# Kernel tuning notes

Hardware: AMD Instinct MI355X
Metric: run time of the kernel (lower is better)

The kernel has to match this reference:

```python
import jax, jax.numpy as jnp
import numpy as np

N = 20000
E = 320000
IN_C, HID, OUT_C = 128, 64, 32
H12, H3 = 4, 1  # heads for conv1/conv2 and conv3
NEG_SLOPE = 0.2


def _glorot(key, shape):
    fan_in, fan_out = shape[0], shape[-1]
    lim = (6.0 / (fan_in + fan_out)) ** 0.5
    return jax.random.uniform(key, shape, jnp.float32, -lim, lim)


def setup_inputs() -> dict:
    key = jax.random.key(0)
    ks = jax.random.split(key, 16)
    x = jax.random.normal(ks[0], (N, IN_C), jnp.float32)
    edge_index = jax.random.randint(ks[1], (2, E), 0, N, jnp.int64)
    p = {
        'W1': _glorot(ks[2], (IN_C, H12 * HID)),
        'as1': _glorot(ks[3], (H12, HID)), 'ad1': _glorot(ks[4], (H12, HID)),
        'b1': jnp.zeros((HID,), jnp.float32),
        'W2': _glorot(ks[5], (HID, H12 * HID)),
        'as2': _glorot(ks[6], (H12, HID)), 'ad2': _glorot(ks[7], (H12, HID)),
        'b2': jnp.zeros((HID,), jnp.float32),
        'W3': _glorot(ks[8], (HID, H3 * OUT_C)),
        'as3': _glorot(ks[9], (H3, OUT_C)), 'ad3': _glorot(ks[10], (H3, OUT_C)),
        'b3': jnp.zeros((OUT_C,), jnp.float32),
        'Wm': _glorot(ks[11], (OUT_C, OUT_C)), 'bm': jnp.zeros((OUT_C,), jnp.float32),
        'Wv': _glorot(ks[12], (OUT_C, OUT_C)), 'bv': jnp.zeros((OUT_C,), jnp.float32),
    }
    return dict(x=x, edge_index=edge_index, **p)


def gat_layer(x, src, dst, W, a_src, a_dst, b, heads, out_c):
    # x: [N, in_c] -> h: [N, H, C]
    h = (x @ W).reshape(-1, heads, out_c)
    alpha_s = jnp.einsum('nhc,hc->nh', h, a_src)  # [N,H]
    alpha_d = jnp.einsum('nhc,hc->nh', h, a_dst)
    e = jax.nn.leaky_relu(alpha_s[src] + alpha_d[dst], NEG_SLOPE)  # [E',H]
    # segment softmax over incoming edges of each dst node
    m = jax.ops.segment_max(e, dst, num_segments=N)
    p = jnp.exp(e - m[dst])
    s = jax.ops.segment_sum(p, dst, num_segments=N)
    alpha = p / (s[dst] + 1e-16)  # [E',H]
    msg = h[src] * alpha[:, :, None]  # [E',H,C]
    out = jax.ops.segment_sum(msg, dst, num_segments=N)  # [N,H,C]
    return out.mean(axis=1) + b  # concat=False -> mean over heads


def reference(x, edge_index, W1, as1, ad1, b1, W2, as2, ad2, b2,
              W3, as3, ad3, b3, Wm, bm, Wv, bv):
    # PyG GATConv default: add self loops
    loop = jnp.arange(N, dtype=edge_index.dtype)
    src = jnp.concatenate([edge_index[0], loop])
    dst = jnp.concatenate([edge_index[1], loop])

    h = jax.nn.relu(gat_layer(x, src, dst, W1, as1, ad1, b1, H12, HID))
    h = jax.nn.relu(gat_layer(h, src, dst, W2, as2, ad2, b2, H12, HID))
    z = gat_layer(h, src, dst, W3, as3, ad3, b3, H3, OUT_C)

    z_mean = z @ Wm + bm
    z_var = jnp.clip(jnp.exp(z @ Wv + bv), 1e-8, 100.0)
    return (z_mean, z_var, z)
```

## Files before the change

kernel.cpp:

```cpp
#include <hip/hip_runtime.h>
#include <hip/hip_bf16.h>

typedef unsigned short ushortT;
typedef short short8 __attribute__((ext_vector_type(8)));
typedef unsigned short ushort8v __attribute__((ext_vector_type(8)));
typedef float float4v __attribute__((ext_vector_type(4)));

constexpr int Nn   = 20000;
constexpr int Ee   = 320000;
constexpr int EP   = Ee + Nn;
constexpr float NSL = 0.2f;
constexpr int CAP  = 128;

__device__ __forceinline__ float b2f(__hip_bfloat16 v) { return __bfloat162float(v); }
__device__ __forceinline__ float bits2f(unsigned short u) {
    __hip_bfloat16 b; *(unsigned short*)&b = u; return __bfloat162float(b);
}
__device__ __forceinline__ unsigned short f2bits(float v) {
    __hip_bfloat16 b = __float2bfloat16(v); return *(unsigned short*)&b;
}
__device__ __forceinline__ float ldf(const void* p, size_t i, int bf) {
    return bf ? __bfloat162float(((const __hip_bfloat16*)p)[i])
              : ((const float*)p)[i];
}
__device__ __forceinline__ void stf(void* p, size_t i, float v, int bf) {
    if (bf) ((__hip_bfloat16*)p)[i] = __float2bfloat16(v);
    else    ((float*)p)[i] = v;
}

__device__ __forceinline__ int local_bf(const unsigned* __restrict__ xbits, int* c_sh) {
    int c = 0;
    for (int i = threadIdx.x; i < 512; i += 256) {
        unsigned e = (xbits[i] >> 7) & 0xFFu;
        if (e >= 110u && e <= 135u) ++c;
    }
    atomicAdd(c_sh, c);
    __syncthreads();
    return (*c_sh > 384) ? 1 : 0;
}

__global__ void setup_k(const int* __restrict__ ei, const unsigned* __restrict__ xbits,
                        int* __restrict__ eflag, int* __restrict__ fflag,
                        int* __restrict__ cnt,
                        const void* __restrict__ W1, const void* __restrict__ W2,
                        ushortT* __restrict__ WT1, ushortT* __restrict__ WT2) {
    const int b = blockIdx.x;
    if (b < 79) {
        int gi = b * 256 + threadIdx.x;
        if (gi < Nn) cnt[gi] = 0;
        if (b == 0) {
            __shared__ int bad, c_s;
            if (threadIdx.x == 0) { bad = 0; c_s = 0; }
            __syncthreads();
            for (int i = threadIdx.x; i < 1024; i += 256)
                if (ei[2 * i + 1] != 0) bad = 1;
            int bf = local_bf(xbits, &c_s);
            __syncthreads();
            if (threadIdx.x == 0) {
                *eflag = bad ? 0 : 1;
                *fflag = bf;
            }
        }
        return;
    }
    __shared__ int c_s;
    if (threadIdx.x == 0) c_s = 0;
    __syncthreads();
    const int bf = local_bf(xbits, &c_s);
    int idx = (b - 79) * 256 + threadIdx.x;
    if (idx < 256 * 128) {
        int j = idx >> 7, k = idx & 127;
        WT1[idx] = f2bits(ldf(W1, (size_t)k * 256 + j, bf));
    } else {
        int i2 = idx - 256 * 128;
        if (i2 < 256 * 64) {
            int j = i2 >> 6, k = i2 & 63;
            WT2[i2] = f2bits(ldf(W2, (size_t)k * 256 + j, bf));
        }
    }
}

__device__ __forceinline__ void load_edge(const int* __restrict__ ei, int sh, int e,
                                          int& si, int& di) {
    if (e < Ee) {
        si = ei[(size_t)e << sh];
        di = ei[(size_t)(Ee + e) << sh];
    } else {
        si = di = e - Ee;
    }
}

__global__ void scatter_k(const int* __restrict__ ei, const int* __restrict__ eflag,
                          int* __restrict__ cnt, int* __restrict__ csr) {
    int e = blockIdx.x * 256 + threadIdx.x;
    if (e >= EP) return;
    int sh = *eflag, si, di;
    load_edge(ei, sh, e, si, di);
    int pos = atomicAdd(cnt + di, 1);
    if (pos < CAP) csr[di * CAP + pos] = si;
}

template <int XMODE, int INC>
__global__ __launch_bounds__(256) void gemm_mfma(const void* __restrict__ xg,
                                                 const ushortT* __restrict__ WT,
                                                 ushortT* __restrict__ h,
                                                 const void* __restrict__ avs,
                                                 const void* __restrict__ avd,
                                                 float* __restrict__ as_, float* __restrict__ ad_,
                                                 const int* __restrict__ fflag) {
    constexpr int SW = INC + 8, SX = INC + 8, CPR = INC / 8;
    const int bf  = *fflag;
    const int xbf = (XMODE == 0) ? bf : 1;
    __shared__ ushortT wt_s[128 * SW];
    __shared__ ushortT xs[64 * SX];
    __shared__ float av_s[2][128];
    const int base = blockIdx.x * 64;
    const int jh   = blockIdx.y;
    const ushortT* WTg = WT + (size_t)jh * 128 * INC;
    for (int ch = threadIdx.x; ch < 128 * CPR; ch += 256) {
        int j = ch / CPR, kc = (ch - j * CPR) * 8;
        *(short8*)(wt_s + j * SW + kc) = *(const short8*)(WTg + j * INC + kc);
    }
    for (int ch = threadIdx.x; ch < 64 * CPR; ch += 256) {
        int nl = ch / CPR, kc = (ch - nl * CPR) * 8;
        int node = base + nl;
        short8 v = {0, 0, 0, 0, 0, 0, 0, 0};
        if (node < Nn) {
            if (xbf) {
                v = *(const short8*)((const ushortT*)xg + (size_t)node * INC + kc);
            } else {
                const float* xf = (const float*)xg + (size_t)node * INC + kc;
#pragma unroll
                for (int i = 0; i < 8; ++i) v[i] = (short)f2bits(xf[i]);
            }
        }
        *(short8*)(xs + nl * SX + kc) = v;
    }
    if (threadIdx.x < 128) {
        av_s[0][threadIdx.x] = ldf(avs, jh * 128 + threadIdx.x, bf);
        av_s[1][threadIdx.x] = ldf(avd, jh * 128 + threadIdx.x, bf);
    }
    __syncthreads();
    const int lane = threadIdx.x & 63, w = threadIdx.x >> 6;
    const int ln = lane & 15, quad = lane >> 4;
    float4v acc[8];
#pragma unroll
    for (int T = 0; T < 8; ++T) acc[T] = (float4v){0.f, 0.f, 0.f, 0.f};
#pragma unroll
    for (int ks = 0; ks < INC / 32; ++ks) {
        const int kb = ks * 32 + quad * 8;
        const short8 b = *(const short8*)(xs + (w * 16 + ln) * SX + kb);
#pragma unroll
        for (int T = 0; T < 8; ++T) {
            const short8 a = *(const short8*)(wt_s + (T * 16 + ln) * SW + kb);
            acc[T] = __builtin_amdgcn_mfma_f32_16x16x32_bf16(a, b, acc[T], 0, 0, 0);
        }
    }
    const int node = base + w * 16 + ln;
    const bool live = (node < Nn);
    ushortT* hn = h + (size_t)node * 256 + jh * 128;
    float pas0 = 0, pas1 = 0, pad0 = 0, pad1 = 0;
#pragma unroll
    for (int T = 0; T < 8; ++T) {
        const int jl = T * 16 + quad * 4;
        ushort4 pk;
        pk.x = f2bits(acc[T][0]); pk.y = f2bits(acc[T][1]);
        pk.z = f2bits(acc[T][2]); pk.w = f2bits(acc[T][3]);
        if (live) *(ushort4*)(hn + jl) = pk;
#pragma unroll
        for (int r = 0; r < 4; ++r) {
            const float v = acc[T][r];
            const float was = av_s[0][jl + r], wad = av_s[1][jl + r];
            if (T < 4) { pas0 = fmaf(v, was, pas0); pad0 = fmaf(v, wad, pad0); }
            else       { pas1 = fmaf(v, was, pas1); pad1 = fmaf(v, wad, pad1); }
        }
    }
#pragma unroll
    for (int off = 16; off < 64; off <<= 1) {
        pas0 += __shfl_xor(pas0, off, 64);
        pas1 += __shfl_xor(pas1, off, 64);
        pad0 += __shfl_xor(pad0, off, 64);
        pad1 += __shfl_xor(pad1, off, 64);
    }
    if (lane < 16 && live) {
        as_[node * 4 + jh * 2]     = pas0;
        as_[node * 4 + jh * 2 + 1] = pas1;
        ad_[node * 4 + jh * 2]     = pad0;
        ad_[node * 4 + jh * 2 + 1] = pad1;
    }
}

__global__ __launch_bounds__(256) void gemm_small(const ushortT* __restrict__ x,
                                                  const void* __restrict__ W,
                                                  __hip_bfloat16* __restrict__ h,
                                                  const void* __restrict__ avs,
                                                  const void* __restrict__ avd,
                                                  float* __restrict__ as_, float* __restrict__ ad_,
                                                  const int* __restrict__ fflag, int N) {
    constexpr int INC = 64, R = 32, PAD = R + 4;
    const int bf = *fflag;
    __shared__ float xsh[INC * PAD];
    int base = blockIdx.x * R;
    for (int i = threadIdx.x; i < R * INC; i += 256) {
        int rr = i / INC, kk = i - rr * INC;
        int nn = base + rr;
        xsh[kk * PAD + rr] = (nn < N) ? bits2f(x[(size_t)nn * INC + kk]) : 0.0f;
    }
    __syncthreads();
    const int jc = threadIdx.x & 31;
    const int g  = threadIdx.x >> 5;
    float acc[4] = {};
    if (bf) {
        const __hip_bfloat16* Wb = (const __hip_bfloat16*)W;
#pragma unroll 4
        for (int k = 0; k < INC; ++k) {
            float4 xv = *(const float4*)(xsh + k * PAD + g * 4);
            float w = b2f(Wb[k * 32 + jc]);
            acc[0] = fmaf(xv.x, w, acc[0]);
            acc[1] = fmaf(xv.y, w, acc[1]);
            acc[2] = fmaf(xv.z, w, acc[2]);
            acc[3] = fmaf(xv.w, w, acc[3]);
        }
    } else {
        const float* Wf = (const float*)W;
#pragma unroll 4
        for (int k = 0; k < INC; ++k) {
            float4 xv = *(const float4*)(xsh + k * PAD + g * 4);
            float w = Wf[k * 32 + jc];
            acc[0] = fmaf(xv.x, w, acc[0]);
            acc[1] = fmaf(xv.y, w, acc[1]);
            acc[2] = fmaf(xv.z, w, acc[2]);
            acc[3] = fmaf(xv.w, w, acc[3]);
        }
    }
    float avsr = ldf(avs, jc, bf), avdr = ldf(avd, jc, bf);
#pragma unroll
    for (int m = 0; m < 4; ++m) {
        int n = base + g * 4 + m;
        if (n >= N) continue;
        h[(size_t)n * 32 + jc] = __float2bfloat16(acc[m]);
        float t1 = acc[m] * avsr;
        float t2 = acc[m] * avdr;
#pragma unroll
        for (int off = 16; off > 0; off >>= 1) {
            t1 += __shfl_down(t1, off, 32);
            t2 += __shfl_down(t2, off, 32);
        }
        if (jc == 0) { as_[n] = t1; ad_[n] = t2; }
    }
}

__global__ __launch_bounds__(256) void aggr4_k(const int* __restrict__ cnt,
                                               const int* __restrict__ csr,
                                               const float* __restrict__ as_,
                                               const float* __restrict__ ad_,
                                               const unsigned short* __restrict__ h,
                                               const void* __restrict__ bias,
                                               const int* __restrict__ fflag,
                                               ushortT* __restrict__ outB, int N) {
    __shared__ float lal[4][CAP][4];
    const int lane = threadIdx.x & 63, seg = threadIdx.x >> 6;
    int d = blockIdx.x * 4 + seg;
    if (d >= N) d = N - 1;
    const int deg = min(cnt[d], CAP);
    const int base = d * CAP;
    const float4 adv = *(const float4*)(ad_ + d * 4);
    const int src0 = (lane < deg) ? csr[base + lane] : 0;
    const int src1 = (64 + lane < deg) ? csr[base + 64 + lane] : 0;
    float s0 = 0, s1 = 0, s2 = 0, s3 = 0;
    if (lane < deg) {
        float4 av = *(const float4*)(as_ + src0 * 4);
        float v0 = av.x + adv.x; v0 = v0 > 0.f ? v0 : NSL * v0; float e0 = __expf(v0);
        float v1 = av.y + adv.y; v1 = v1 > 0.f ? v1 : NSL * v1; float e1 = __expf(v1);
        float v2 = av.z + adv.z; v2 = v2 > 0.f ? v2 : NSL * v2; float e2 = __expf(v2);
        float v3 = av.w + adv.w; v3 = v3 > 0.f ? v3 : NSL * v3; float e3 = __expf(v3);
        s0 += e0; s1 += e1; s2 += e2; s3 += e3;
        *(float4*)(&lal[seg][lane][0]) = make_float4(e0, e1, e2, e3);
    }
    if (64 + lane < deg) {
        float4 av = *(const float4*)(as_ + src1 * 4);
        float v0 = av.x + adv.x; v0 = v0 > 0.f ? v0 : NSL * v0; float e0 = __expf(v0);
        float v1 = av.y + adv.y; v1 = v1 > 0.f ? v1 : NSL * v1; float e1 = __expf(v1);
        float v2 = av.z + adv.z; v2 = v2 > 0.f ? v2 : NSL * v2; float e2 = __expf(v2);
        float v3 = av.w + adv.w; v3 = v3 > 0.f ? v3 : NSL * v3; float e3 = __expf(v3);
        s0 += e0; s1 += e1; s2 += e2; s3 += e3;
        *(float4*)(&lal[seg][64 + lane][0]) = make_float4(e0, e1, e2, e3);
    }
    const int hl = lane >> 5, cl = lane & 31;
    const int q = cl >> 3, c8 = (cl & 7) * 8;
    const float* lal_s = &lal[seg][0][0];
    float a[8] = {0, 0, 0, 0, 0, 0, 0, 0};

    auto do_edge = [&](int idx, bool valid) {
        int sa = __shfl(src0, idx & 63, 64);
        int sb = __shfl(src1, idx & 63, 64);
        int src = (idx < 64) ? sa : sb;
        float ev = valid ? lal_s[idx * 4 + q] : 0.0f;
        int off = valid ? src * 256 : 0;
        ushort8v hv = *(const ushort8v*)(h + off + q * 64 + c8);
#pragma unroll
        for (int i = 0; i < 8; ++i) a[i] = fmaf(ev, bits2f(hv[i]), a[i]);
    };

    int e = 0;
    for (; e + 8 <= deg; e += 8) {
        do_edge(e + hl, true);
        do_edge(e + 2 + hl, true);
        do_edge(e + 4 + hl, true);
        do_edge(e + 6 + hl, true);
    }
    for (; e < deg; e += 2) do_edge(e + hl, (e + hl) < deg);

#pragma unroll
    for (int off = 1; off < 64; off <<= 1) {
        s0 += __shfl_xor(s0, off, 64);
        s1 += __shfl_xor(s1, off, 64);
        s2 += __shfl_xor(s2, off, 64);
        s3 += __shfl_xor(s3, off, 64);
    }
    const float sq = (q == 0) ? s0 : (q == 1) ? s1 : (q == 2) ? s2 : s3;
    const float iq = 0.25f / (sq + 1e-16f);
#pragma unroll
    for (int i = 0; i < 8; ++i) {
        a[i] *= iq;
        a[i] += __shfl_xor(a[i], 32, 64);
        a[i] += __shfl_xor(a[i], 8, 64);
        a[i] += __shfl_xor(a[i], 16, 64);
    }
    if (lane < 8) {
        const int bf = *fflag;
        ushort8v p;
#pragma unroll
        for (int i = 0; i < 8; ++i) {
            float r = fmaxf(a[i] + ldf(bias, lane * 8 + i, bf), 0.f);
            p[i] = f2bits(r);
        }
        *(ushort8v*)(outB + (size_t)d * 64 + lane * 8) = p;
    }
}

__global__ __launch_bounds__(256) void aggr1f_k(const int* __restrict__ cnt,
                                                const int* __restrict__ csr,
                                                const float* __restrict__ as_,
                                                const float* __restrict__ ad_,
                                                const ushortT* __restrict__ h,
                                                const void* __restrict__ b3,
                                                const void* __restrict__ Wm,
                                                const void* __restrict__ bm,
                                                const void* __restrict__ Wv,
                                                const void* __restrict__ bv,
                                                const int* __restrict__ fflag,
                                                void* __restrict__ out, int N) {
    __shared__ float wm_s[1024], wv_s[1024];
    __shared__ float lal[8][CAP];
    __shared__ int   lof[8][CAP];
    const int bf = *fflag;
    for (int i = threadIdx.x; i < 1024; i += 256) {
        wm_s[i] = ldf(Wm, i, bf);
        wv_s[i] = ldf(Wv, i, bf);
    }
    __syncthreads();
    const int c = threadIdx.x & 31, seg = threadIdx.x >> 5;
    const int d = blockIdx.x * 8 + seg;
    if (d >= N) return;
    const int deg = min(cnt[d], CAP);
    const int base = d * CAP;
    const float advd = ad_[d];
    float s = 0;
    for (int i = c; i < deg; i += 32) {
        int src = csr[base + i];
        float v = as_[src] + advd;
        v = v > 0.f ? v : NSL * v;
        float ev = __expf(v);
        s += ev;
        lal[seg][i] = ev;
        lof[seg][i] = src * 32;
    }
    float acc = 0.0f;
    int e = 0;
    for (; e + 4 <= deg; e += 4) {
        float ev0 = lal[seg][e], ev1 = lal[seg][e + 1];
        float ev2 = lal[seg][e + 2], ev3 = lal[seg][e + 3];
        int o0 = lof[seg][e], o1 = lof[seg][e + 1];
        int o2 = lof[seg][e + 2], o3 = lof[seg][e + 3];
        float h0 = bits2f(h[o0 + c]), h1 = bits2f(h[o1 + c]);
        float h2 = bits2f(h[o2 + c]), h3 = bits2f(h[o3 + c]);
        acc = fmaf(ev0, h0, acc);
        acc = fmaf(ev1, h1, acc);
        acc = fmaf(ev2, h2, acc);
        acc = fmaf(ev3, h3, acc);
    }
    for (; e < deg; ++e) acc = fmaf(lal[seg][e], bits2f(h[lof[seg][e] + c]), acc);
#pragma unroll
    for (int off = 1; off < 32; off <<= 1) s += __shfl_xor(s, off, 32);
    const float inv = 1.0f / (s + 1e-16f);
    const float z = inv * acc + ldf(b3, c, bf);
    stf(out, (size_t)2 * N * 32 + (size_t)d * 32 + c, z, bf);
    float sm = ldf(bm, c, bf), sv = ldf(bv, c, bf);
#pragma unroll 8
    for (int k = 0; k < 32; ++k) {
        float zk = __shfl(z, k, 32);
        sm = fmaf(zk, wm_s[k * 32 + c], sm);
        sv = fmaf(zk, wv_s[k * 32 + c], sv);
    }
    float var = __expf(sv);
    var = fminf(fmaxf(var, 1e-8f), 100.0f);
    stf(out, (size_t)d * 32 + c, sm, bf);
    stf(out, (size_t)N * 32 + (size_t)d * 32 + c, var, bf);
}

extern "C" void kernel_launch(void* const* d_in, const int* in_sizes, int n_in,
                              void* d_out, int out_size, void* d_ws, size_t ws_size,
                              hipStream_t stream) {
    const void* x   = d_in[0];
    const int*  ei  = (const int*)d_in[1];
    const void* W1  = d_in[2];
    const void* as1 = d_in[3];
    const void* ad1 = d_in[4];
    const void* b1  = d_in[5];
    const void* W2  = d_in[6];
    const void* as2 = d_in[7];
    const void* ad2 = d_in[8];
    const void* b2  = d_in[9];
    const void* W3  = d_in[10];
    const void* as3 = d_in[11];
    const void* ad3 = d_in[12];
    const void* b3  = d_in[13];
    const void* Wm  = d_in[14];
    const void* bm  = d_in[15];
    const void* Wv  = d_in[16];
    const void* bv  = d_in[17];

    float* ws = (float*)d_ws;
    ushortT* h    = (ushortT*)ws;
    ushortT* x1b  = (ushortT*)(ws + 2560000);
    ushortT* x2b  = (ushortT*)(ws + 3200000);
    float*  as_   = ws + 3840000;
    float*  ad_   = ws + 3920000;
    ushortT* WT1  = (ushortT*)(ws + 4000000);
    ushortT* WT2  = (ushortT*)(ws + 4016384);
    int*    cnt   = (int*)(ws + 4024576);
    int*    csr   = (int*)(ws + 4044576);
    int*    eflag = (int*)(ws + 6604576);
    int*    fflag = (int*)(ws + 6604577);

    setup_k<<<271, 256, 0, stream>>>(ei, (const unsigned*)x, eflag, fflag, cnt,
                                     W1, W2, WT1, WT2);
    scatter_k<<<(EP + 255) / 256, 256, 0, stream>>>(ei, eflag, cnt, csr);

    dim3 gg(313, 2);
    gemm_mfma<0, 128><<<gg, 256, 0, stream>>>(x, WT1, h, as1, ad1, as_, ad_, fflag);
    aggr4_k<<<5000, 256, 0, stream>>>(cnt, csr, as_, ad_, h, b1, fflag, x1b, Nn);

    gemm_mfma<1, 64><<<gg, 256, 0, stream>>>(x1b, WT2, h, as2, ad2, as_, ad_, fflag);
    aggr4_k<<<5000, 256, 0, stream>>>(cnt, csr, as_, ad_, h, b2, fflag, x2b, Nn);

    gemm_small<<<625, 256, 0, stream>>>(x2b, W3, (__hip_bfloat16*)h, as3, ad3, as_, ad_, fflag, Nn);
    aggr1f_k<<<2500, 256, 0, stream>>>(cnt, csr, as_, ad_, h,
                                       b3, Wm, bm, Wv, bv, fflag, d_out, Nn);
}
```

Before: 217.2 us.

## Aggregate raw inputs before projection and fold attention vectors into weights

```diff
diff --git a/kernel.cpp b/kernel.cpp
--- a/kernel.cpp
+++ b/kernel.cpp
@@ -43,7 +43,10 @@
                         int* __restrict__ eflag, int* __restrict__ fflag,
                         int* __restrict__ cnt,
                         const void* __restrict__ W1, const void* __restrict__ W2,
-                        ushortT* __restrict__ WT1, ushortT* __restrict__ WT2) {
+                        const void* __restrict__ as1, const void* __restrict__ ad1,
+                        const void* __restrict__ as2, const void* __restrict__ ad2,
+                        ushortT* __restrict__ WT1c, ushortT* __restrict__ WT2c,
+                        float* __restrict__ wp1, float* __restrict__ wp2) {
     const int b = blockIdx.x;
     if (b < 79) {
         int gi = b * 256 + threadIdx.x;
@@ -67,15 +70,35 @@
     if (threadIdx.x == 0) c_s = 0;
     __syncthreads();
     const int bf = local_bf(xbits, &c_s);
-    int idx = (b - 79) * 256 + threadIdx.x;
-    if (idx < 256 * 128) {
-        int j = idx >> 7, k = idx & 127;
-        WT1[idx] = f2bits(ldf(W1, (size_t)k * 256 + j, bf));
+    if (b < 271) {
+        int idx = (b - 79) * 256 + threadIdx.x;
+        if (idx < 64 * 512) {
+            int jp = idx >> 9, r = idx & 511, hh = r >> 7, k = r & 127;
+            WT1c[idx] = f2bits(ldf(W1, (size_t)k * 256 + hh * 64 + jp, bf));
+        } else {
+            int i2 = idx - 64 * 512;
+            int jp = i2 >> 8, r = i2 & 255, hh = r >> 6, k = r & 63;
+            WT2c[i2] = f2bits(ldf(W2, (size_t)k * 256 + hh * 64 + jp, bf));
+        }
     } else {
-        int i2 = idx - 256 * 128;
-        if (i2 < 256 * 64) {
-            int j = i2 >> 6, k = i2 & 63;
-            WT2[i2] = f2bits(ldf(W2, (size_t)k * 256 + j, bf));
+        int idx = (b - 271) * 256 + threadIdx.x;
+        if (idx < 1024) {
+            int sd = idx >> 9, r = idx & 511, hh = r >> 7, k = r & 127;
+            const void* av = sd ? ad1 : as1;
+            float acc = 0.f;
+            for (int c = 0; c < 64; ++c)
+                acc = fmaf(ldf(W1, (size_t)k * 256 + hh * 64 + c, bf),
+                           ldf(av, hh * 64 + c, bf), acc);
+            wp1[idx] = acc;
+        } else if (idx < 1536) {
+            int i2 = idx - 1024;
+            int sd = i2 >> 8, r = i2 & 255, hh = r >> 6, k = r & 63;
+            const void* av = sd ? ad2 : as2;
+            float acc = 0.f;
+            for (int c = 0; c < 64; ++c)
+                acc = fmaf(ldf(W2, (size_t)k * 256 + hh * 64 + c, bf),
+                           ldf(av, hh * 64 + c, bf), acc);
+            wp2[i2] = acc;
         }
     }
 }
@@ -100,164 +123,60 @@
     if (pos < CAP) csr[di * CAP + pos] = si;
 }
 
-template <int XMODE, int INC>
-__global__ __launch_bounds__(256) void gemm_mfma(const void* __restrict__ xg,
-                                                 const ushortT* __restrict__ WT,
-                                                 ushortT* __restrict__ h,
-                                                 const void* __restrict__ avs,
-                                                 const void* __restrict__ avd,
-                                                 float* __restrict__ as_, float* __restrict__ ad_,
-                                                 const int* __restrict__ fflag) {
-    constexpr int SW = INC + 8, SX = INC + 8, CPR = INC / 8;
-    const int bf  = *fflag;
-    const int xbf = (XMODE == 0) ? bf : 1;
-    __shared__ ushortT wt_s[128 * SW];
-    __shared__ ushortT xs[64 * SX];
-    __shared__ float av_s[2][128];
-    const int base = blockIdx.x * 64;
-    const int jh   = blockIdx.y;
-    const ushortT* WTg = WT + (size_t)jh * 128 * INC;
-    for (int ch = threadIdx.x; ch < 128 * CPR; ch += 256) {
-        int j = ch / CPR, kc = (ch - j * CPR) * 8;
-        *(short8*)(wt_s + j * SW + kc) = *(const short8*)(WTg + j * INC + kc);
-    }
-    for (int ch = threadIdx.x; ch < 64 * CPR; ch += 256) {
-        int nl = ch / CPR, kc = (ch - nl * CPR) * 8;
-        int node = base + nl;
-        short8 v = {0, 0, 0, 0, 0, 0, 0, 0};
-        if (node < Nn) {
-            if (xbf) {
-                v = *(const short8*)((const ushortT*)xg + (size_t)node * INC + kc);
-            } else {
-                const float* xf = (const float*)xg + (size_t)node * INC + kc;
-#pragma unroll
-                for (int i = 0; i < 8; ++i) v[i] = (short)f2bits(xf[i]);
-            }
-        }
-        *(short8*)(xs + nl * SX + kc) = v;
-    }
-    if (threadIdx.x < 128) {
-        av_s[0][threadIdx.x] = ldf(avs, jh * 128 + threadIdx.x, bf);
-        av_s[1][threadIdx.x] = ldf(avd, jh * 128 + threadIdx.x, bf);
-    }
-    __syncthreads();
-    const int lane = threadIdx.x & 63, w = threadIdx.x >> 6;
-    const int ln = lane & 15, quad = lane >> 4;
-    float4v acc[8];
-#pragma unroll
-    for (int T = 0; T < 8; ++T) acc[T] = (float4v){0.f, 0.f, 0.f, 0.f};
-#pragma unroll
-    for (int ks = 0; ks < INC / 32; ++ks) {
-        const int kb = ks * 32 + quad * 8;
-        const short8 b = *(const short8*)(xs + (w * 16 + ln) * SX + kb);
-#pragma unroll
-        for (int T = 0; T < 8; ++T) {
-            const short8 a = *(const short8*)(wt_s + (T * 16 + ln) * SW + kb);
-            acc[T] = __builtin_amdgcn_mfma_f32_16x16x32_bf16(a, b, acc[T], 0, 0, 0);
-        }
-    }
-    const int node = base + w * 16 + ln;
-    const bool live = (node < Nn);
-    ushortT* hn = h + (size_t)node * 256 + jh * 128;
-    float pas0 = 0, pas1 = 0, pad0 = 0, pad1 = 0;
-#pragma unroll
-    for (int T = 0; T < 8; ++T) {
-        const int jl = T * 16 + quad * 4;
-        ushort4 pk;
-        pk.x = f2bits(acc[T][0]); pk.y = f2bits(acc[T][1]);
-        pk.z = f2bits(acc[T][2]); pk.w = f2bits(acc[T][3]);
-        if (live) *(ushort4*)(hn + jl) = pk;
-#pragma unroll
-        for (int r = 0; r < 4; ++r) {
-            const float v = acc[T][r];
-            const float was = av_s[0][jl + r], wad = av_s[1][jl + r];
-            if (T < 4) { pas0 = fmaf(v, was, pas0); pad0 = fmaf(v, wad, pad0); }
-            else       { pas1 = fmaf(v, was, pas1); pad1 = fmaf(v, wad, pad1); }
-        }
-    }
-#pragma unroll
-    for (int off = 16; off < 64; off <<= 1) {
-        pas0 += __shfl_xor(pas0, off, 64);
-        pas1 += __shfl_xor(pas1, off, 64);
-        pad0 += __shfl_xor(pad0, off, 64);
-        pad1 += __shfl_xor(pad1, off, 64);
-    }
-    if (lane < 16 && live) {
-        as_[node * 4 + jh * 2]     = pas0;
-        as_[node * 4 + jh * 2 + 1] = pas1;
-        ad_[node * 4 + jh * 2]     = pad0;
-        ad_[node * 4 + jh * 2 + 1] = pad1;
-    }
-}
-
-__global__ __launch_bounds__(256) void gemm_small(const ushortT* __restrict__ x,
-                                                  const void* __restrict__ W,
-                                                  __hip_bfloat16* __restrict__ h,
-                                                  const void* __restrict__ avs,
-                                                  const void* __restrict__ avd,
-                                                  float* __restrict__ as_, float* __restrict__ ad_,
-                                                  const int* __restrict__ fflag, int N) {
-    constexpr int INC = 64, R = 32, PAD = R + 4;
+__global__ __launch_bounds__(256) void alpha1_k(const void* __restrict__ xg,
+                                                const float* __restrict__ wp1,
+                                                ushortT* __restrict__ xb,
+                                                float* __restrict__ as_,
+                                                float* __restrict__ ad_,
+                                                const int* __restrict__ fflag, int N) {
     const int bf = *fflag;
-    __shared__ float xsh[INC * PAD];
-    int base = blockIdx.x * R;
-    for (int i = threadIdx.x; i < R * INC; i += 256) {
-        int rr = i / INC, kk = i - rr * INC;
-        int nn = base + rr;
-        xsh[kk * PAD + rr] = (nn < N) ? bits2f(x[(size_t)nn * INC + kk]) : 0.0f;
-    }
-    __syncthreads();
-    const int jc = threadIdx.x & 31;
-    const int g  = threadIdx.x >> 5;
-    float acc[4] = {};
+    const int cl = threadIdx.x & 31, g = threadIdx.x >> 5;
+    const int n = blockIdx.x * 8 + g;
+    if (n >= N) return;
+    const int c4 = cl * 4;
+    float xv[4];
     if (bf) {
-        const __hip_bfloat16* Wb = (const __hip_bfloat16*)W;
-#pragma unroll 4
-        for (int k = 0; k < INC; ++k) {
-            float4 xv = *(const float4*)(xsh + k * PAD + g * 4);
-            float w = b2f(Wb[k * 32 + jc]);
-            acc[0] = fmaf(xv.x, w, acc[0]);
-            acc[1] = fmaf(xv.y, w, acc[1]);
-            acc[2] = fmaf(xv.z, w, acc[2]);
-            acc[3] = fmaf(xv.w, w, acc[3]);
-        }
+        ushort4 u = *(const ushort4*)((const ushortT*)xg + (size_t)n * 128 + c4);
+        xv[0] = bits2f(u.x); xv[1] = bits2f(u.y); xv[2] = bits2f(u.z); xv[3] = bits2f(u.w);
+        *(ushort4*)(xb + (size_t)n * 128 + c4) = u;
     } else {
-        const float* Wf = (const float*)W;
-#pragma unroll 4
-        for (int k = 0; k < INC; ++k) {
-            float4 xv = *(const float4*)(xsh + k * PAD + g * 4);
-            float w = Wf[k * 32 + jc];
-            acc[0] = fmaf(xv.x, w, acc[0]);
-            acc[1] = fmaf(xv.y, w, acc[1]);
-            acc[2] = fmaf(xv.z, w, acc[2]);
-            acc[3] = fmaf(xv.w, w, acc[3]);
-        }
-    }
-    float avsr = ldf(avs, jc, bf), avdr = ldf(avd, jc, bf);
-#pragma unroll
-    for (int m = 0; m < 4; ++m) {
-        int n = base + g * 4 + m;
-        if (n >= N) continue;
-        h[(size_t)n * 32 + jc] = __float2bfloat16(acc[m]);
-        float t1 = acc[m] * avsr;
-        float t2 = acc[m] * avdr;
-#pragma unroll
-        for (int off = 16; off > 0; off >>= 1) {
-            t1 += __shfl_down(t1, off, 32);
-            t2 += __shfl_down(t2, off, 32);
-        }
-        if (jc == 0) { as_[n] = t1; ad_[n] = t2; }
-    }
-}
-
-__global__ __launch_bounds__(256) void aggr4_k(const int* __restrict__ cnt,
-                                               const int* __restrict__ csr,
-                                               const float* __restrict__ as_,
-                                               const float* __restrict__ ad_,
-                                               const unsigned short* __restrict__ h,
-                                               const void* __restrict__ bias,
-                                               const int* __restrict__ fflag,
-                                               ushortT* __restrict__ outB, int N) {
+        float4 f = *(const float4*)((const float*)xg + (size_t)n * 128 + c4);
+        xv[0] = f.x; xv[1] = f.y; xv[2] = f.z; xv[3] = f.w;
+        ushort4 u;
+        u.x = f2bits(f.x); u.y = f2bits(f.y); u.z = f2bits(f.z); u.w = f2bits(f.w);
+        *(ushort4*)(xb + (size_t)n * 128 + c4) = u;
+    }
+    float p[8];
+#pragma unroll
+    for (int j = 0; j < 8; ++j) {
+        float4 wv = *(const float4*)(wp1 + j * 128 + c4);
+        float t = 0.f;
+        t = fmaf(xv[0], wv.x, t);
+        t = fmaf(xv[1], wv.y, t);
+        t = fmaf(xv[2], wv.z, t);
+        t = fmaf(xv[3], wv.w, t);
+        p[j] = t;
+    }
+#pragma unroll
+    for (int off = 1; off < 32; off <<= 1) {
+#pragma unroll
+        for (int j = 0; j < 8; ++j) p[j] += __shfl_xor(p[j], off, 32);
+    }
+    if (cl == 0) {
+        *(float4*)(as_ + (size_t)n * 4) = make_float4(p[0], p[1], p[2], p[3]);
+        *(float4*)(ad_ + (size_t)n * 4) = make_float4(p[4], p[5], p[6], p[7]);
+    }
+}
+
+template <int CIN>
+__global__ __launch_bounds__(256) void aggx_k(const int* __restrict__ cnt,
+                                              const int* __restrict__ csr,
+                                              const float* __restrict__ as_,
+                                              const float* __restrict__ ad_,
+                                              const ushortT* __restrict__ xb,
+                                              ushortT* __restrict__ aggn, int N) {
+    constexpr int LPE = CIN / 8;
+    constexpr int EPW = 64 / LPE;
     __shared__ float lal[4][CAP][4];
     const int lane = threadIdx.x & 63, seg = threadIdx.x >> 6;
     int d = blockIdx.x * 4 + seg;
@@ -286,30 +205,41 @@
         s0 += e0; s1 += e1; s2 += e2; s3 += e3;
         *(float4*)(&lal[seg][64 + lane][0]) = make_float4(e0, e1, e2, e3);
     }
-    const int hl = lane >> 5, cl = lane & 31;
-    const int q = cl >> 3, c8 = (cl & 7) * 8;
+    const int EL = lane / LPE;
+    const int c8 = (lane & (LPE - 1)) * 8;
     const float* lal_s = &lal[seg][0][0];
-    float a[8] = {0, 0, 0, 0, 0, 0, 0, 0};
+    float a[4][8];
+#pragma unroll
+    for (int h = 0; h < 4; ++h)
+#pragma unroll
+        for (int j = 0; j < 8; ++j) a[h][j] = 0.f;
 
     auto do_edge = [&](int idx, bool valid) {
         int sa = __shfl(src0, idx & 63, 64);
         int sb = __shfl(src1, idx & 63, 64);
         int src = (idx < 64) ? sa : sb;
-        float ev = valid ? lal_s[idx * 4 + q] : 0.0f;
-        int off = valid ? src * 256 : 0;
-        ushort8v hv = *(const ushort8v*)(h + off + q * 64 + c8);
-#pragma unroll
-        for (int i = 0; i < 8; ++i) a[i] = fmaf(ev, bits2f(hv[i]), a[i]);
+        int ii = valid ? idx : 0;
+        float4 ev = *(const float4*)(lal_s + ii * 4);
+        float g = valid ? 1.f : 0.f;
+        int off = valid ? src * CIN : 0;
+        ushort8v xv = *(const ushort8v*)(xb + (size_t)off + c8);
+        float ex0 = ev.x * g, ex1 = ev.y * g, ex2 = ev.z * g, ex3 = ev.w * g;
+#pragma unroll
+        for (int j = 0; j < 8; ++j) {
+            float xf = bits2f(xv[j]);
+            a[0][j] = fmaf(ex0, xf, a[0][j]);
+            a[1][j] = fmaf(ex1, xf, a[1][j]);
+            a[2][j] = fmaf(ex2, xf, a[2][j]);
+            a[3][j] = fmaf(ex3, xf, a[3][j]);
+        }
     };
 
     int e = 0;
-    for (; e + 8 <= deg; e += 8) {
-        do_edge(e + hl, true);
-        do_edge(e + 2 + hl, true);
-        do_edge(e + 4 + hl, true);
-        do_edge(e + 6 + hl, true);
-    }
-    for (; e < deg; e += 2) do_edge(e + hl, (e + hl) < deg);
+    for (; e + 2 * EPW <= deg; e += 2 * EPW) {
+        do_edge(e + EL, true);
+        do_edge(e + EPW + EL, true);
+    }
+    for (; e < deg; e += EPW) do_edge(e + EL, (e + EL) < deg);
 
 #pragma unroll
     for (int off = 1; off < 64; off <<= 1) {
@@ -318,24 +248,178 @@
         s2 += __shfl_xor(s2, off, 64);
         s3 += __shfl_xor(s3, off, 64);
     }
-    const float sq = (q == 0) ? s0 : (q == 1) ? s1 : (q == 2) ? s2 : s3;
-    const float iq = 0.25f / (sq + 1e-16f);
-#pragma unroll
-    for (int i = 0; i < 8; ++i) {
-        a[i] *= iq;
-        a[i] += __shfl_xor(a[i], 32, 64);
-        a[i] += __shfl_xor(a[i], 8, 64);
-        a[i] += __shfl_xor(a[i], 16, 64);
-    }
-    if (lane < 8) {
-        const int bf = *fflag;
-        ushort8v p;
-#pragma unroll
-        for (int i = 0; i < 8; ++i) {
-            float r = fmaxf(a[i] + ldf(bias, lane * 8 + i, bf), 0.f);
-            p[i] = f2bits(r);
-        }
-        *(ushort8v*)(outB + (size_t)d * 64 + lane * 8) = p;
+#pragma unroll
+    for (int h = 0; h < 4; ++h)
+#pragma unroll
+        for (int j = 0; j < 8; ++j) {
+#pragma unroll
+            for (int off2 = LPE; off2 < 64; off2 <<= 1)
+                a[h][j] += __shfl_xor(a[h][j], off2, 64);
+        }
+    if (EL == 0) {
+        const float i0 = 0.25f / (s0 + 1e-16f);
+        const float i1 = 0.25f / (s1 + 1e-16f);
+        const float i2 = 0.25f / (s2 + 1e-16f);
+        const float i3 = 0.25f / (s3 + 1e-16f);
+        ushortT* op = aggn + (size_t)d * (4 * CIN) + c8;
+        ushort8v p0, p1, p2, p3;
+#pragma unroll
+        for (int j = 0; j < 8; ++j) {
+            p0[j] = f2bits(a[0][j] * i0);
+            p1[j] = f2bits(a[1][j] * i1);
+            p2[j] = f2bits(a[2][j] * i2);
+            p3[j] = f2bits(a[3][j] * i3);
+        }
+        *(ushort8v*)(op + 0 * CIN) = p0;
+        *(ushort8v*)(op + 1 * CIN) = p1;
+        *(ushort8v*)(op + 2 * CIN) = p2;
+        *(ushort8v*)(op + 3 * CIN) = p3;
+    }
+}
+
+template <int K, int NPROJ>
+__global__ __launch_bounds__(256) void gemm_cat(const ushortT* __restrict__ aggn,
+                                                const ushortT* __restrict__ WTc,
+                                                const void* __restrict__ bias,
+                                                const float* __restrict__ wp,
+                                                ushortT* __restrict__ xout,
+                                                float* __restrict__ as_,
+                                                float* __restrict__ ad_,
+                                                const int* __restrict__ fflag, int N) {
+    constexpr int KC = 128, SW = KC + 8, NCH = K / KC;
+    const int bf = *fflag;
+    __shared__ ushortT wt_s[64 * SW];
+    __shared__ ushortT xs[64 * SW];
+    __shared__ float wp_s[512];
+    const int base = blockIdx.x * 64;
+    const int lane = threadIdx.x & 63, w = threadIdx.x >> 6;
+    const int ln = lane & 15, quad = lane >> 4;
+    float4v acc[4];
+#pragma unroll
+    for (int T = 0; T < 4; ++T) acc[T] = (float4v){0.f, 0.f, 0.f, 0.f};
+    if (NPROJ) {
+        for (int i = threadIdx.x; i < NPROJ * 64; i += 256) wp_s[i] = wp[i];
+    }
+#pragma unroll
+    for (int ch = 0; ch < NCH; ++ch) {
+        for (int i = threadIdx.x; i < 64 * 16; i += 256) {
+            int r = i >> 4, kc = (i & 15) * 8;
+            *(short8*)(wt_s + r * SW + kc) =
+                *(const short8*)(WTc + (size_t)r * K + ch * KC + kc);
+            int node = base + r;
+            short8 v = {0, 0, 0, 0, 0, 0, 0, 0};
+            if (node < N) v = *(const short8*)(aggn + (size_t)node * K + ch * KC + kc);
+            *(short8*)(xs + r * SW + kc) = v;
+        }
+        __syncthreads();
+#pragma unroll
+        for (int ks = 0; ks < 4; ++ks) {
+            const int kb = ks * 32 + quad * 8;
+            const short8 bfr = *(const short8*)(xs + (w * 16 + ln) * SW + kb);
+#pragma unroll
+            for (int T = 0; T < 4; ++T) {
+                const short8 afr = *(const short8*)(wt_s + (T * 16 + ln) * SW + kb);
+                acc[T] = __builtin_amdgcn_mfma_f32_16x16x32_bf16(afr, bfr, acc[T], 0, 0, 0);
+            }
+        }
+        __syncthreads();
+    }
+    const int node = base + w * 16 + ln;
+    const bool live = node < N;
+    ushortT* on = xout + (size_t)node * 64;
+    float p[8];
+#pragma unroll
+    for (int j = 0; j < 8; ++j) p[j] = 0.f;
+#pragma unroll
+    for (int T = 0; T < 4; ++T) {
+        const int jl = T * 16 + quad * 4;
+        ushort4 pk;
+        float t0 = fmaxf(acc[T][0] + ldf(bias, jl + 0, bf), 0.f);
+        float t1 = fmaxf(acc[T][1] + ldf(bias, jl + 1, bf), 0.f);
+        float t2 = fmaxf(acc[T][2] + ldf(bias, jl + 2, bf), 0.f);
+        float t3 = fmaxf(acc[T][3] + ldf(bias, jl + 3, bf), 0.f);
+        pk.x = f2bits(t0); pk.y = f2bits(t1); pk.z = f2bits(t2); pk.w = f2bits(t3);
+        if (live) *(ushort4*)(on + jl) = pk;
+        if (NPROJ) {
+#pragma unroll
+            for (int j = 0; j < 8; ++j) {
+                p[j] = fmaf(t0, wp_s[j * 64 + jl + 0], p[j]);
+                p[j] = fmaf(t1, wp_s[j * 64 + jl + 1], p[j]);
+                p[j] = fmaf(t2, wp_s[j * 64 + jl + 2], p[j]);
+                p[j] = fmaf(t3, wp_s[j * 64 + jl + 3], p[j]);
+            }
+        }
+    }
+    if (NPROJ) {
+#pragma unroll
+        for (int j = 0; j < 8; ++j) {
+            p[j] += __shfl_xor(p[j], 16, 64);
+            p[j] += __shfl_xor(p[j], 32, 64);
+        }
+        if (quad == 0 && live) {
+            *(float4*)(as_ + (size_t)node * 4) = make_float4(p[0], p[1], p[2], p[3]);
+            *(float4*)(ad_ + (size_t)node * 4) = make_float4(p[4], p[5], p[6], p[7]);
+        }
+    }
+}
+
+__global__ __launch_bounds__(256) void gemm_small(const ushortT* __restrict__ x,
+                                                  const void* __restrict__ W,
+                                                  __hip_bfloat16* __restrict__ h,
+                                                  const void* __restrict__ avs,
+                                                  const void* __restrict__ avd,
+                                                  float* __restrict__ as_, float* __restrict__ ad_,
+                                                  const int* __restrict__ fflag, int N) {
+    constexpr int INC = 64, R = 32, PAD = R + 4;
+    const int bf = *fflag;
+    __shared__ float xsh[INC * PAD];
+    int base = blockIdx.x * R;
+    for (int i = threadIdx.x; i < R * INC; i += 256) {
+        int rr = i / INC, kk = i - rr * INC;
+        int nn = base + rr;
+        xsh[kk * PAD + rr] = (nn < N) ? bits2f(x[(size_t)nn * INC + kk]) : 0.0f;
+    }
+    __syncthreads();
+    const int jc = threadIdx.x & 31;
+    const int g  = threadIdx.x >> 5;
+    float acc[4] = {};
+    if (bf) {
+        const __hip_bfloat16* Wb = (const __hip_bfloat16*)W;
+#pragma unroll 4
+        for (int k = 0; k < INC; ++k) {
+            float4 xv = *(const float4*)(xsh + k * PAD + g * 4);
+            float w = b2f(Wb[k * 32 + jc]);
+            acc[0] = fmaf(xv.x, w, acc[0]);
+            acc[1] = fmaf(xv.y, w, acc[1]);
+            acc[2] = fmaf(xv.z, w, acc[2]);
+            acc[3] = fmaf(xv.w, w, acc[3]);
+        }
+    } else {
+        const float* Wf = (const float*)W;
+#pragma unroll 4
+        for (int k = 0; k < INC; ++k) {
+            float4 xv = *(const float4*)(xsh + k * PAD + g * 4);
+            float w = Wf[k * 32 + jc];
+            acc[0] = fmaf(xv.x, w, acc[0]);
+            acc[1] = fmaf(xv.y, w, acc[1]);
+            acc[2] = fmaf(xv.z, w, acc[2]);
+            acc[3] = fmaf(xv.w, w, acc[3]);
+        }
+    }
+    float avsr = ldf(avs, jc, bf), avdr = ldf(avd, jc, bf);
+#pragma unroll
+    for (int m = 0; m < 4; ++m) {
+        int n = base + g * 4 + m;
+        if (n >= N) continue;
+        h[(size_t)n * 32 + jc] = __float2bfloat16(acc[m]);
+        float t1 = acc[m] * avsr;
+        float t2 = acc[m] * avdr;
+#pragma unroll
+        for (int off = 16; off > 0; off >>= 1) {
+            t1 += __shfl_down(t1, off, 32);
+            t2 += __shfl_down(t2, off, 32);
+        }
+        if (jc == 0) { as_[n] = t1; ad_[n] = t2; }
     }
 }
 
@@ -432,30 +516,34 @@
     const void* bv  = d_in[17];
 
     float* ws = (float*)d_ws;
-    ushortT* h    = (ushortT*)ws;
-    ushortT* x1b  = (ushortT*)(ws + 2560000);
-    ushortT* x2b  = (ushortT*)(ws + 3200000);
-    float*  as_   = ws + 3840000;
-    float*  ad_   = ws + 3920000;
-    ushortT* WT1  = (ushortT*)(ws + 4000000);
-    ushortT* WT2  = (ushortT*)(ws + 4016384);
-    int*    cnt   = (int*)(ws + 4024576);
-    int*    csr   = (int*)(ws + 4044576);
-    int*    eflag = (int*)(ws + 6604576);
-    int*    fflag = (int*)(ws + 6604577);
-
-    setup_k<<<271, 256, 0, stream>>>(ei, (const unsigned*)x, eflag, fflag, cnt,
-                                     W1, W2, WT1, WT2);
+    ushortT* aggn = (ushortT*)ws;
+    ushortT* xb   = (ushortT*)(ws + 5120000);
+    ushortT* x1b  = (ushortT*)(ws + 6400000);
+    ushortT* x2b  = (ushortT*)(ws + 7040000);
+    ushortT* h3   = (ushortT*)(ws + 7680000);
+    float*  as_   = ws + 8000000;
+    float*  ad_   = ws + 8080000;
+    ushortT* WT1c = (ushortT*)(ws + 8160000);
+    ushortT* WT2c = (ushortT*)(ws + 8176384);
+    float*  wp1   = ws + 8184576;
+    float*  wp2   = ws + 8185600;
+    int*    cnt   = (int*)(ws + 8186112);
+    int*    csr   = (int*)(ws + 8206112);
+    int*    eflag = (int*)(ws + 10766112);
+    int*    fflag = (int*)(ws + 10766113);
+
+    setup_k<<<277, 256, 0, stream>>>(ei, (const unsigned*)x, eflag, fflag, cnt,
+                                     W1, W2, as1, ad1, as2, ad2, WT1c, WT2c, wp1, wp2);
     scatter_k<<<(EP + 255) / 256, 256, 0, stream>>>(ei, eflag, cnt, csr);
 
-    dim3 gg(313, 2);
-    gemm_mfma<0, 128><<<gg, 256, 0, stream>>>(x, WT1, h, as1, ad1, as_, ad_, fflag);
-    aggr4_k<<<5000, 256, 0, stream>>>(cnt, csr, as_, ad_, h, b1, fflag, x1b, Nn);
-
-    gemm_mfma<1, 64><<<gg, 256, 0, stream>>>(x1b, WT2, h, as2, ad2, as_, ad_, fflag);
-    aggr4_k<<<5000, 256, 0, stream>>>(cnt, csr, as_, ad_, h, b2, fflag, x2b, Nn);
-
-    gemm_small<<<625, 256, 0, stream>>>(x2b, W3, (__hip_bfloat16*)h, as3, ad3, as_, ad_, fflag, Nn);
-    aggr1f_k<<<2500, 256, 0, stream>>>(cnt, csr, as_, ad_, h,
+    alpha1_k<<<2500, 256, 0, stream>>>(x, wp1, xb, as_, ad_, fflag, Nn);
+    aggx_k<128><<<5000, 256, 0, stream>>>(cnt, csr, as_, ad_, xb, aggn, Nn);
+    gemm_cat<512, 8><<<313, 256, 0, stream>>>(aggn, WT1c, b1, wp2, x1b, as_, ad_, fflag, Nn);
+
+    aggx_k<64><<<5000, 256, 0, stream>>>(cnt, csr, as_, ad_, x1b, aggn, Nn);
+    gemm_cat<256, 0><<<313, 256, 0, stream>>>(aggn, WT2c, b2, nullptr, x2b, as_, ad_, fflag, Nn);
+
+    gemm_small<<<625, 256, 0, stream>>>(x2b, W3, (__hip_bfloat16*)h3, as3, ad3, as_, ad_, fflag, Nn);
+    aggr1f_k<<<2500, 256, 0, stream>>>(cnt, csr, as_, ad_, h3,
                                        b3, Wm, bm, Wv, bv, fflag, d_out, Nn);
 }
```

Result: slower. 243.1 us (+11.9%).
